# Kernel optimization log

Hardware: AMD Instinct MI355X
Metric: run time of the kernel (lower is better)

## Reference

```python
import jax, jax.numpy as jnp
import numpy as np

CENTER_EXTEND_PX = 3.0  # center_extend_px
SIGMA = 2.0             # center_gt_blur
KSIZE = 21              # GaussianLayer: ReflectionPad2d(10) + 21x21 depthwise gaussian
PAD = KSIZE // 2


def _gaussian_kernel():
    ax = np.arange(KSIZE, dtype=np.float64) - PAD
    xx, yy = np.meshgrid(ax, ax)
    g = np.exp(-(xx ** 2 + yy ** 2) / (2.0 * SIGMA ** 2))
    g /= g.sum()
    return jnp.asarray(g, dtype=jnp.float32)


def _blur(x, kernel):
    # x: [H, W]; reflect-pad then VALID depthwise conv == GaussianLayer
    xp = jnp.pad(x, PAD, mode='reflect')
    return jax.lax.conv_general_dilated(xp[None, None], kernel[None, None], (1, 1), 'VALID')[0, 0]


def setup_inputs():
    key = jax.random.key(0)
    B, N, H, W = 4, 64, 512, 512
    kc = jax.random.fold_in(key, 1)
    # centers[b, n] = (y, x) pixel coordinates; >0 means valid
    centers = jax.random.randint(kc, (B, N, 2), 1, min(H, W)).astype(jnp.float32)
    centerdir_gt = jnp.zeros((B, 6, H, W), dtype=jnp.float32)
    return {"centers": centers, "centerdir_gt": centerdir_gt, "kernel": _gaussian_kernel()}


def reference(centers, centerdir_gt, kernel):
    B, _, H, W = centerdir_gt.shape
    # xym grid: xym[0] varies along width, xym[1] varies along height (integer coords)
    grid_h = jnp.arange(H, dtype=jnp.float32)[:, None]  # xym[1]: [H,1]
    grid_w = jnp.arange(W, dtype=jnp.float32)[None, :]  # xym[0]: [1,W]

    def per_item(c, gt_b):
        valid = (c[:, 0] > 0) | (c[:, 1] > 0)          # [N]
        cy, cx = c[:, 0], c[:, 1]
        # original: X = xym[1] (height grid) paired with center_x = centers[:,1]
        dx = grid_h[:, :, None] - cx                    # [H,1,N]
        dy = grid_w[:, :, None] - cy                    # [1,W,N]
        d2 = dx * dx + dy * dy                          # [H,W,N]; squared dist (same argmin as sqrt)
        d2 = jnp.where(valid[None, None, :], d2, jnp.inf)
        ids = jnp.argmin(d2, axis=-1)                   # [H,W] nearest valid center per pixel
        gt_X = cx[ids] - grid_h                         # [H,W]
        gt_Y = cy[ids] - grid_w
        r2 = gt_X * gt_X + gt_Y * gt_Y
        gt_R = jnp.where(r2 > 0, jnp.sqrt(jnp.where(r2 > 0, r2, 1.0)), 0.0)
        gt_theta = jnp.arctan2(gt_Y, jnp.where(r2 > 0, gt_X, 1.0))  # atan2(0,1)=0 == atan2(0,0)
        s, co = jnp.sin(gt_theta), jnp.cos(gt_theta)
        M = jnp.sqrt(s * s + co * co)
        s, co = s / M, co / M
        near = (jnp.abs(gt_X) < CENTER_EXTEND_PX) & (jnp.abs(gt_Y) < CENTER_EXTEND_PX)
        has_valid = valid.any()
        mask0 = jnp.where(has_valid, near.astype(jnp.float32), 0.0)  # == 1 - gt_center_mask
        blurred = _blur(mask0, kernel)
        m = blurred.max()
        center_mask = jnp.where(mask0.max() > 0, blurred / jnp.maximum(m, 1e-12), 0.0)
        ch = jnp.where(has_valid, jnp.stack([gt_R, gt_theta, s, co]), gt_b[:4])
        return jnp.concatenate([ch, gt_b[4:5], center_mask[None]], axis=0)  # [6,H,W]

    return jax.vmap(per_item)(centers, centerdir_gt)
```

## Files before the change

### kernel.cpp

```cpp
#include <hip/hip_runtime.h>
#include <math.h>
#include <limits.h>

namespace {
constexpr int BB   = 4;
constexpr int NCH  = 6;
constexpr int HH   = 512;
constexpr int WW   = 512;
constexpr int NCEN = 64;
constexpr int KSZ  = 21;
constexpr int PADR = 10;
constexpr int HW   = HH * WW;
constexpr int BOXSTRIDE = 640;

__device__ __forceinline__ int refl(int q, int n) {
    q = (q < 0) ? -q : q;
    q = (q >= n) ? (2 * n - 2 - q) : q;
    return q;
}

__global__ __launch_bounds__(256) void k_geom(
    const float* __restrict__ centers,
    const float* __restrict__ gt,
    float* __restrict__ out,
    float* __restrict__ mask,
    unsigned int* __restrict__ maxbuf)
{
    __shared__ float s_cxf[NCEN], s_cyf[NCEN];
    __shared__ int   s_kx[NCEN], s_ky8[NCEN], s_ki[NCEN];
    __shared__ int   s_cnt, s_hasv;

    const int b    = blockIdx.y;
    const int tid  = threadIdx.x;
    const int tIdx = blockIdx.x;
    const int r0   = (tIdx >> 4) * 32;
    const int c0   = (tIdx & 15) * 32;

    if (tIdx == 0 && tid == 0) maxbuf[b] = 0u;

    if (tid < NCEN) {
        float cy = centers[(b * NCEN + tid) * 2 + 0];
        float cx = centers[(b * NCEN + tid) * 2 + 1];
        bool valid = (cy > 0.0f) || (cx > 0.0f);
        s_cxf[tid] = cx;
        s_cyf[tid] = cy;
        float r0f = (float)r0, r1f = (float)(r0 + 31);
        float c0f = (float)c0, c1f = (float)(c0 + 31);
        float drm = fmaxf(fmaxf(r0f - cx, cx - r1f), 0.0f);
        float dcm = fmaxf(fmaxf(c0f - cy, cy - c1f), 0.0f);
        float drM = fmaxf(cx - r0f, r1f - cx);
        float dcM = fmaxf(cy - c0f, c1f - cy);
        float mind2 = drm * drm + dcm * dcm;
        float maxd2 = drM * drM + dcM * dcM;
        if (!valid) { mind2 = __int_as_float(0x7f800000); maxd2 = mind2; }
        float ub = maxd2;
#pragma unroll
        for (int off = 32; off > 0; off >>= 1)
            ub = fminf(ub, __shfl_xor(ub, off, 64));
        bool keep = valid && (mind2 <= ub);
        unsigned long long km = __ballot(keep);
        unsigned long long vm = __ballot(valid);
        if (keep) {
            int pos = __popcll(km & ((1ull << tid) - 1ull));
            s_kx[pos]  = (int)cx;
            s_ky8[pos] = ((int)cy) * 8;
            s_ki[pos]  = tid;
        }
        if (tid == 0) { s_cnt = (int)__popcll(km); s_hasv = (vm != 0ull) ? 1 : 0; }
    }
    __syncthreads();

    const int row = r0 + (tid >> 3);
    const int wb  = c0 + (tid & 7) * 4;
    const int w8  = wb * 8;
    const int cnt = s_cnt;
    const bool hv = (s_hasv != 0);

    int b0 = INT_MAX, b1 = INT_MAX, b2 = INT_MAX, b3 = INT_MAX;
    for (int k = 0; k < cnt; ++k) {
        int dr   = row - s_kx[k];
        int base = (__mul24(dr, dr) << 6) + s_ki[k];
        int icy8 = s_ky8[k];
        int d0 = w8      - icy8; b0 = min(b0, __mul24(d0, d0) + base);
        int d1 = w8 + 8  - icy8; b1 = min(b1, __mul24(d1, d1) + base);
        int d2 = w8 + 16 - icy8; b2 = min(b2, __mul24(d2, d2) + base);
        int d3 = w8 + 24 - icy8; b3 = min(b3, __mul24(d3, d3) + base);
    }
    int bi[4] = { b0 & 63, b1 & 63, b2 & 63, b3 & 63 };

    float aR[4], aT[4], aS[4], aC[4], aM[4];
    const float fh = (float)row;
#pragma unroll
    for (int j = 0; j < 4; ++j) {
        float cxw = s_cxf[bi[j]];
        float cyw = s_cyf[bi[j]];
        float gX = cxw - fh;
        float gY = cyw - (float)(wb + j);
        float r2 = gX * gX + gY * gY;
        bool rpos = r2 > 0.0f;
        float R = rpos ? sqrtf(r2) : 0.0f;
        aR[j] = R;
        aT[j] = atan2f(gY, rpos ? gX : 1.0f);
        float invR = rpos ? (1.0f / R) : 0.0f;
        aS[j] = rpos ? gY * invR : 0.0f;
        aC[j] = rpos ? gX * invR : 1.0f;
        bool nearc = (fabsf(gX) < 3.0f) && (fabsf(gY) < 3.0f);
        aM[j] = (hv && nearc) ? 1.0f : 0.0f;
    }

    const size_t base = (size_t)b * NCH * HW + (size_t)(row * WW + wb);
    if (hv) {
        *(float4*)&out[base + 0 * (size_t)HW] = make_float4(aR[0], aR[1], aR[2], aR[3]);
        *(float4*)&out[base + 1 * (size_t)HW] = make_float4(aT[0], aT[1], aT[2], aT[3]);
        *(float4*)&out[base + 2 * (size_t)HW] = make_float4(aS[0], aS[1], aS[2], aS[3]);
        *(float4*)&out[base + 3 * (size_t)HW] = make_float4(aC[0], aC[1], aC[2], aC[3]);
    } else {
        *(float4*)&out[base + 0 * (size_t)HW] = *(const float4*)&gt[base + 0 * (size_t)HW];
        *(float4*)&out[base + 1 * (size_t)HW] = *(const float4*)&gt[base + 1 * (size_t)HW];
        *(float4*)&out[base + 2 * (size_t)HW] = *(const float4*)&gt[base + 2 * (size_t)HW];
        *(float4*)&out[base + 3 * (size_t)HW] = *(const float4*)&gt[base + 3 * (size_t)HW];
    }
    *(float4*)&out[base + 4 * (size_t)HW] = *(const float4*)&gt[base + 4 * (size_t)HW];
    *(float4*)&out[base + 5 * (size_t)HW] = make_float4(0.f, 0.f, 0.f, 0.f);
    *(float4*)&mask[(size_t)b * HW + (size_t)(row * WW + wb)] =
        make_float4(aM[0], aM[1], aM[2], aM[3]);
}

__device__ __forceinline__ void load_k1(const float* __restrict__ g2d, float* k1) {
    if (threadIdx.x < KSZ) {
        float s = 0.0f;
#pragma unroll
        for (int j = 0; j < KSZ; ++j) s += g2d[threadIdx.x * KSZ + j];
        k1[threadIdx.x] = s;
    }
}

__global__ __launch_bounds__(256) void k_blur_sparse(
    const float* __restrict__ centers,
    const float* __restrict__ mask,
    const float* __restrict__ g2d,
    float* __restrict__ blurbox,
    unsigned int* __restrict__ maxbuf)
{
    const int b  = blockIdx.y;
    const int ci = blockIdx.x;
    float cy = centers[(b * NCEN + ci) * 2 + 0];
    float cx = centers[(b * NCEN + ci) * 2 + 1];
    if (!((cy > 0.0f) || (cx > 0.0f))) return;
    const int icx = (int)cx, icy = (int)cy;
    const int rA = max(icx - 12, 0), rB = min(icx + 12, HH - 1);
    const int cA = max(icy - 12, 0), cB = min(icy + 12, WW - 1);
    const int pr0 = max(rA - PADR, 0), pr1 = min(rB + PADR, HH - 1);
    const int pc0 = max(cA - PADR, 0), pc1 = min(cB + PADR, WW - 1);
    const int nr = pr1 - pr0 + 1, nc = pc1 - pc0 + 1;
    const int nh = rB - rA + 1,  nw = cB - cA + 1;

    __shared__ float k1[KSZ];
    __shared__ float patch[45 * 48];
    __shared__ float tmp[25 * 46];
    load_k1(g2d, k1);

    const float* mb = mask + (size_t)b * HW;
    for (int e = threadIdx.x; e < nr * nc; e += 256) {
        int r = e / nc, c = e - r * nc;
        patch[r * 48 + c] = mb[(pr0 + r) * WW + (pc0 + c)];
    }
    __syncthreads();

    for (int e = threadIdx.x; e < nh * nc; e += 256) {
        int lr = e / nc, j = e - lr * nc;
        int r  = rA + lr;
        float acc = 0.0f;
#pragma unroll
        for (int dv = -PADR; dv <= PADR; ++dv) {
            int q = refl(r + dv, HH);
            acc = fmaf(k1[dv + PADR], patch[(q - pr0) * 48 + j], acc);
        }
        tmp[lr * 46 + j] = acc;
    }
    __syncthreads();

    float vmax = 0.0f;
    float* bx = blurbox + (size_t)(b * NCEN + ci) * BOXSTRIDE;
    for (int e = threadIdx.x; e < nh * nw; e += 256) {
        int lr = e / nw, j = e - lr * nw;
        int w  = cA + j;
        float acc = 0.0f;
#pragma unroll
        for (int d = -PADR; d <= PADR; ++d) {
            int q = refl(w + d, WW);
            acc = fmaf(k1[d + PADR], tmp[lr * 46 + (q - pc0)], acc);
        }
        bx[lr * 25 + j] = acc;
        vmax = fmaxf(vmax, acc);
    }
#pragma unroll
    for (int off = 32; off > 0; off >>= 1)
        vmax = fmaxf(vmax, __shfl_down(vmax, off, 64));
    __shared__ float swr[4];
    const int lane = threadIdx.x & 63, wid = threadIdx.x >> 6;
    if (lane == 0) swr[wid] = vmax;
    __syncthreads();
    if (threadIdx.x == 0) {
        float m = fmaxf(fmaxf(swr[0], swr[1]), fmaxf(swr[2], swr[3]));
        atomicMax(&maxbuf[b], __float_as_uint(m));
    }
}

__global__ __launch_bounds__(256) void k_norm_sparse(
    const float* __restrict__ centers,
    const float* __restrict__ blurbox,
    const unsigned int* __restrict__ maxbuf,
    float* __restrict__ out)
{
    const int b  = blockIdx.y;
    const int ci = blockIdx.x;
    float cy = centers[(b * NCEN + ci) * 2 + 0];
    float cx = centers[(b * NCEN + ci) * 2 + 1];
    if (!((cy > 0.0f) || (cx > 0.0f))) return;
    const int icx = (int)cx, icy = (int)cy;
    const int rA = max(icx - 12, 0), rB = min(icx + 12, HH - 1);
    const int cA = max(icy - 12, 0), cB = min(icy + 12, WW - 1);
    const int nh = rB - rA + 1, nw = cB - cA + 1;

    const float inv = 1.0f / fmaxf(__uint_as_float(maxbuf[b]), 1e-12f);
    const float* bx = blurbox + (size_t)(b * NCEN + ci) * BOXSTRIDE;
    float* o5 = out + ((size_t)b * NCH + 5) * HW;
    for (int e = threadIdx.x; e < nh * nw; e += 256) {
        int lr = e / nw, j = e - lr * nw;
        o5[(rA + lr) * WW + (cA + j)] = bx[lr * 25 + j] * inv;
    }
}

}

extern "C" void kernel_launch(void* const* d_in, const int* in_sizes, int n_in,
                              void* d_out, int out_size, void* d_ws, size_t ws_size,
                              hipStream_t stream) {
    (void)in_sizes; (void)n_in; (void)out_size; (void)ws_size;
    const float* centers = (const float*)d_in[0];
    const float* gt      = (const float*)d_in[1];
    const float* g2d     = (const float*)d_in[2];
    float* out  = (float*)d_out;
    float* mask = (float*)d_ws;
    float* blurbox = (float*)d_ws + (size_t)BB * HW;
    unsigned int* maxbuf =
        (unsigned int*)((float*)d_ws + (size_t)BB * HW + (size_t)BB * NCEN * BOXSTRIDE);

    dim3 gridG(256, BB);
    k_geom<<<gridG, 256, 0, stream>>>(centers, gt, out, mask, maxbuf);
    dim3 gridS(NCEN, BB);
    k_blur_sparse<<<gridS, 256, 0, stream>>>(centers, mask, g2d, blurbox, maxbuf);
    k_norm_sparse<<<gridS, 256, 0, stream>>>(centers, blurbox, maxbuf, out);
}
```

Before: 95.23 us.

## Fuse sparse blur and normalize kernels via last-block ticket per batch

Merges the sparse blur kernel and the normalization kernel into one launch. Each block does its blur and max reduction, then takes a per-batch ticket with an atomic counter, and the last block to finish normalizes and writes all 64 boxes for that batch. This removes one kernel launch and its launch gap. In exchange, the normalization pass for each batch now runs serially inside a single block, which lengthens the tail of the kernel.

```diff
diff --git a/kernel.cpp b/kernel.cpp
--- a/kernel.cpp
+++ b/kernel.cpp
@@ -24,7 +24,8 @@
     const float* __restrict__ gt,
     float* __restrict__ out,
     float* __restrict__ mask,
-    unsigned int* __restrict__ maxbuf)
+    unsigned int* __restrict__ maxbuf,
+    unsigned int* __restrict__ done)
 {
     __shared__ float s_cxf[NCEN], s_cyf[NCEN];
     __shared__ int   s_kx[NCEN], s_ky8[NCEN], s_ki[NCEN];
@@ -36,7 +37,7 @@
     const int r0   = (tIdx >> 4) * 32;
     const int c0   = (tIdx & 15) * 32;
 
-    if (tIdx == 0 && tid == 0) maxbuf[b] = 0u;
+    if (tIdx == 0 && tid == 0) { maxbuf[b] = 0u; done[b] = 0u; }
 
     if (tid < NCEN) {
         float cy = centers[(b * NCEN + tid) * 2 + 0];
@@ -126,109 +127,112 @@
         make_float4(aM[0], aM[1], aM[2], aM[3]);
 }
 
-__device__ __forceinline__ void load_k1(const float* __restrict__ g2d, float* k1) {
-    if (threadIdx.x < KSZ) {
-        float s = 0.0f;
-#pragma unroll
-        for (int j = 0; j < KSZ; ++j) s += g2d[threadIdx.x * KSZ + j];
-        k1[threadIdx.x] = s;
-    }
-}
-
-__global__ __launch_bounds__(256) void k_blur_sparse(
+__global__ __launch_bounds__(256) void k_blurnorm(
     const float* __restrict__ centers,
     const float* __restrict__ mask,
     const float* __restrict__ g2d,
     float* __restrict__ blurbox,
-    unsigned int* __restrict__ maxbuf)
+    unsigned int* __restrict__ maxbuf,
+    unsigned int* __restrict__ done,
+    float* __restrict__ out)
 {
-    const int b  = blockIdx.y;
-    const int ci = blockIdx.x;
+    const int b   = blockIdx.y;
+    const int ci  = blockIdx.x;
+    const int tid = threadIdx.x;
     float cy = centers[(b * NCEN + ci) * 2 + 0];
     float cx = centers[(b * NCEN + ci) * 2 + 1];
-    if (!((cy > 0.0f) || (cx > 0.0f))) return;
-    const int icx = (int)cx, icy = (int)cy;
-    const int rA = max(icx - 12, 0), rB = min(icx + 12, HH - 1);
-    const int cA = max(icy - 12, 0), cB = min(icy + 12, WW - 1);
-    const int pr0 = max(rA - PADR, 0), pr1 = min(rB + PADR, HH - 1);
-    const int pc0 = max(cA - PADR, 0), pc1 = min(cB + PADR, WW - 1);
-    const int nr = pr1 - pr0 + 1, nc = pc1 - pc0 + 1;
-    const int nh = rB - rA + 1,  nw = cB - cA + 1;
+    const bool bvalid = (cy > 0.0f) || (cx > 0.0f);
 
     __shared__ float k1[KSZ];
     __shared__ float patch[45 * 48];
     __shared__ float tmp[25 * 46];
-    load_k1(g2d, k1);
-
-    const float* mb = mask + (size_t)b * HW;
-    for (int e = threadIdx.x; e < nr * nc; e += 256) {
-        int r = e / nc, c = e - r * nc;
-        patch[r * 48 + c] = mb[(pr0 + r) * WW + (pc0 + c)];
-    }
+    __shared__ int   s_ticket;
+
+    if (bvalid) {
+        const int icx = (int)cx, icy = (int)cy;
+        const int rA = max(icx - 12, 0), rB = min(icx + 12, HH - 1);
+        const int cA = max(icy - 12, 0), cB = min(icy + 12, WW - 1);
+        const int pr0 = max(rA - PADR, 0), pr1 = min(rB + PADR, HH - 1);
+        const int pc0 = max(cA - PADR, 0), pc1 = min(cB + PADR, WW - 1);
+        const int nr = pr1 - pr0 + 1, nc = pc1 - pc0 + 1;
+        const int nh = rB - rA + 1,  nw = cB - cA + 1;
+
+        if (tid < KSZ) {
+            float s = 0.0f;
+#pragma unroll
+            for (int j = 0; j < KSZ; ++j) s += g2d[tid * KSZ + j];
+            k1[tid] = s;
+        }
+        const float* mb = mask + (size_t)b * HW;
+        for (int e = tid; e < nr * nc; e += 256) {
+            int r = e / nc, c = e - r * nc;
+            patch[r * 48 + c] = mb[(pr0 + r) * WW + (pc0 + c)];
+        }
+        __syncthreads();
+
+        for (int e = tid; e < nh * nc; e += 256) {
+            int lr = e / nc, j = e - lr * nc;
+            int r  = rA + lr;
+            float acc = 0.0f;
+#pragma unroll
+            for (int dv = -PADR; dv <= PADR; ++dv) {
+                int q = refl(r + dv, HH);
+                acc = fmaf(k1[dv + PADR], patch[(q - pr0) * 48 + j], acc);
+            }
+            tmp[lr * 46 + j] = acc;
+        }
+        __syncthreads();
+
+        float vmax = 0.0f;
+        float* bx = blurbox + (size_t)(b * NCEN + ci) * BOXSTRIDE;
+        for (int e = tid; e < nh * nw; e += 256) {
+            int lr = e / nw, j = e - lr * nw;
+            int w  = cA + j;
+            float acc = 0.0f;
+#pragma unroll
+            for (int d = -PADR; d <= PADR; ++d) {
+                int q = refl(w + d, WW);
+                acc = fmaf(k1[d + PADR], tmp[lr * 46 + (q - pc0)], acc);
+            }
+            bx[lr * 25 + j] = acc;
+            vmax = fmaxf(vmax, acc);
+        }
+#pragma unroll
+        for (int off = 32; off > 0; off >>= 1)
+            vmax = fmaxf(vmax, __shfl_down(vmax, off, 64));
+        __shared__ float swr[4];
+        const int lane = tid & 63, wid = tid >> 6;
+        if (lane == 0) swr[wid] = vmax;
+        __syncthreads();
+        if (tid == 0) {
+            float m = fmaxf(fmaxf(swr[0], swr[1]), fmaxf(swr[2], swr[3]));
+            atomicMax(&maxbuf[b], __float_as_uint(m));
+        }
+        __syncthreads();
+    }
+
+    __threadfence();
+    if (tid == 0) s_ticket = (int)atomicAdd(&done[b], 1u);
     __syncthreads();
-
-    for (int e = threadIdx.x; e < nh * nc; e += 256) {
-        int lr = e / nc, j = e - lr * nc;
-        int r  = rA + lr;
-        float acc = 0.0f;
-#pragma unroll
-        for (int dv = -PADR; dv <= PADR; ++dv) {
-            int q = refl(r + dv, HH);
-            acc = fmaf(k1[dv + PADR], patch[(q - pr0) * 48 + j], acc);
-        }
-        tmp[lr * 46 + j] = acc;
-    }
-    __syncthreads();
-
-    float vmax = 0.0f;
-    float* bx = blurbox + (size_t)(b * NCEN + ci) * BOXSTRIDE;
-    for (int e = threadIdx.x; e < nh * nw; e += 256) {
-        int lr = e / nw, j = e - lr * nw;
-        int w  = cA + j;
-        float acc = 0.0f;
-#pragma unroll
-        for (int d = -PADR; d <= PADR; ++d) {
-            int q = refl(w + d, WW);
-            acc = fmaf(k1[d + PADR], tmp[lr * 46 + (q - pc0)], acc);
-        }
-        bx[lr * 25 + j] = acc;
-        vmax = fmaxf(vmax, acc);
-    }
-#pragma unroll
-    for (int off = 32; off > 0; off >>= 1)
-        vmax = fmaxf(vmax, __shfl_down(vmax, off, 64));
-    __shared__ float swr[4];
-    const int lane = threadIdx.x & 63, wid = threadIdx.x >> 6;
-    if (lane == 0) swr[wid] = vmax;
-    __syncthreads();
-    if (threadIdx.x == 0) {
-        float m = fmaxf(fmaxf(swr[0], swr[1]), fmaxf(swr[2], swr[3]));
-        atomicMax(&maxbuf[b], __float_as_uint(m));
-    }
-}
-
-__global__ __launch_bounds__(256) void k_norm_sparse(
-    const float* __restrict__ centers,
-    const float* __restrict__ blurbox,
-    const unsigned int* __restrict__ maxbuf,
-    float* __restrict__ out)
-{
-    const int b  = blockIdx.y;
-    const int ci = blockIdx.x;
-    float cy = centers[(b * NCEN + ci) * 2 + 0];
-    float cx = centers[(b * NCEN + ci) * 2 + 1];
-    if (!((cy > 0.0f) || (cx > 0.0f))) return;
-    const int icx = (int)cx, icy = (int)cy;
-    const int rA = max(icx - 12, 0), rB = min(icx + 12, HH - 1);
-    const int cA = max(icy - 12, 0), cB = min(icy + 12, WW - 1);
-    const int nh = rB - rA + 1, nw = cB - cA + 1;
-
-    const float inv = 1.0f / fmaxf(__uint_as_float(maxbuf[b]), 1e-12f);
-    const float* bx = blurbox + (size_t)(b * NCEN + ci) * BOXSTRIDE;
+    if (s_ticket != NCEN - 1) return;
+
+    __threadfence();
+    const float inv =
+        1.0f / fmaxf(__uint_as_float(atomicAdd(&maxbuf[b], 0u)), 1e-12f);
     float* o5 = out + ((size_t)b * NCH + 5) * HW;
-    for (int e = threadIdx.x; e < nh * nw; e += 256) {
-        int lr = e / nw, j = e - lr * nw;
-        o5[(rA + lr) * WW + (cA + j)] = bx[lr * 25 + j] * inv;
+    for (int c2 = 0; c2 < NCEN; ++c2) {
+        float cy2 = centers[(b * NCEN + c2) * 2 + 0];
+        float cx2 = centers[(b * NCEN + c2) * 2 + 1];
+        if (!((cy2 > 0.0f) || (cx2 > 0.0f))) continue;
+        const int icx = (int)cx2, icy = (int)cy2;
+        const int rA = max(icx - 12, 0), rB = min(icx + 12, HH - 1);
+        const int cA = max(icy - 12, 0), cB = min(icy + 12, WW - 1);
+        const int nh = rB - rA + 1, nw = cB - cA + 1;
+        const float* bx = blurbox + (size_t)(b * NCEN + c2) * BOXSTRIDE;
+        for (int e = tid; e < nh * nw; e += 256) {
+            int lr = e / nw, j = e - lr * nw;
+            o5[(rA + lr) * WW + (cA + j)] = bx[lr * 25 + j] * inv;
+        }
     }
 }
 
@@ -246,10 +250,10 @@
     float* blurbox = (float*)d_ws + (size_t)BB * HW;
     unsigned int* maxbuf =
         (unsigned int*)((float*)d_ws + (size_t)BB * HW + (size_t)BB * NCEN * BOXSTRIDE);
+    unsigned int* done = maxbuf + BB;
 
     dim3 gridG(256, BB);
-    k_geom<<<gridG, 256, 0, stream>>>(centers, gt, out, mask, maxbuf);
+    k_geom<<<gridG, 256, 0, stream>>>(centers, gt, out, mask, maxbuf, done);
     dim3 gridS(NCEN, BB);
-    k_blur_sparse<<<gridS, 256, 0, stream>>>(centers, mask, g2d, blurbox, maxbuf);
-    k_norm_sparse<<<gridS, 256, 0, stream>>>(centers, blurbox, maxbuf, out);
-}
+    k_blurnorm<<<gridS, 256, 0, stream>>>(centers, mask, g2d, blurbox, maxbuf, done, out);
+}
```

Result: slower. 162.5 us (+70.7%).
